# Optimization experiments

Hardware: AMD Instinct MI355X
Metric: run time of the kernel (lower is better)

Reference implementation:

```python
import jax, jax.numpy as jnp
import numpy as np

HIDDEN = 2048
N_HEADS = 16
HEAD_DIM = HIDDEN // N_HEADS  # 128
BATCH = 2
SEQ = 2048


def setup_inputs() -> dict:
    key = jax.random.key(0)
    ks = jax.random.split(key, 9)
    std = HIDDEN ** -0.5
    inp = {
        "hidden_states": jax.random.normal(ks[0], (BATCH, SEQ, HIDDEN), dtype=jnp.float32),
        "q_w": jax.random.normal(ks[1], (HIDDEN, HIDDEN), dtype=jnp.float32) * std,
        "k_w": jax.random.normal(ks[2], (HIDDEN, HIDDEN), dtype=jnp.float32) * std,
        "v_w": jax.random.normal(ks[3], (HIDDEN, HIDDEN), dtype=jnp.float32) * std,
        "o_w": jax.random.normal(ks[4], (HIDDEN, HIDDEN), dtype=jnp.float32) * std,
        "q_b": jnp.zeros((HIDDEN,), dtype=jnp.float32),
        "k_b": jnp.zeros((HIDDEN,), dtype=jnp.float32),
        "v_b": jnp.zeros((HIDDEN,), dtype=jnp.float32),
        "o_b": jnp.zeros((HIDDEN,), dtype=jnp.float32),
    }
    return inp


def reference(hidden_states, q_w, k_w, v_w, o_w, q_b, k_b, v_b, o_b):
    b, s, _ = hidden_states.shape
    # Projections (nn.Linear applies x @ W^T + b); split heads -> [b, h, s, d]
    def proj(w, bias):
        y = hidden_states @ w.T + bias
        return y.reshape(b, s, N_HEADS, HEAD_DIM).transpose(0, 2, 1, 3)

    q = proj(q_w, q_b)
    k = proj(k_w, k_b)
    v = proj(v_w, v_b)

    scale = 1.0 / jnp.sqrt(jnp.float32(HEAD_DIM))
    scores = jnp.einsum("bhqd,bhkd->bhqk", q, k) * scale  # [b, h, s, s]

    # causal mask: mask positions where k > q (triu, diagonal=1)
    qi = jnp.arange(s)[:, None]
    ki = jnp.arange(s)[None, :]
    scores = jnp.where(ki > qi, -jnp.inf, scores)

    attn = jax.nn.softmax(scores.astype(jnp.float32), axis=-1).astype(q.dtype)
    out = jnp.einsum("bhqk,bhkd->bhqd", attn, v)
    out = out.transpose(0, 2, 1, 3).reshape(b, s, HIDDEN)
    return out @ o_w.T + o_b
```

## Files before the change

### kernel.cpp

```cpp
#include <hip/hip_runtime.h>

#define S_HID 2048
#define S_SEQ 2048
#define S_B   2
#define S_NH  16
#define S_HD  128
#define S_M   (S_B * S_SEQ)
#define S_BH  (S_B * S_NH)

typedef __bf16 bf16_t;
typedef __bf16 bf16x8 __attribute__((ext_vector_type(8)));
typedef __bf16 bf16x4 __attribute__((ext_vector_type(4)));
typedef float  floatx4 __attribute__((ext_vector_type(4)));

typedef __attribute__((address_space(1))) unsigned int as1_uint;
typedef __attribute__((address_space(3))) unsigned int as3_uint;

__device__ __forceinline__ void gload_lds16(const void* g, void* l) {
    __builtin_amdgcn_global_load_lds((as1_uint*)g, (as3_uint*)l, 16, 0, 0);
}

__global__ void cvt_bf16(const float* __restrict__ src, bf16_t* __restrict__ dst, int n) {
    int nv = n >> 2;
    int stride = gridDim.x * blockDim.x;
    for (int i = blockIdx.x * blockDim.x + threadIdx.x; i < nv; i += stride) {
        float4 v = ((const float4*)src)[i];
        bf16x4 o;
        o.x = (bf16_t)v.x; o.y = (bf16_t)v.y; o.z = (bf16_t)v.z; o.w = (bf16_t)v.w;
        ((bf16x4*)dst)[i] = o;
    }
}

__global__ void transpose_v(const bf16_t* __restrict__ V, bf16_t* __restrict__ Vt) {
    __shared__ bf16_t tile[64 * 65];
    const int bh = blockIdx.z, s0 = blockIdx.y * 64, d0 = blockIdx.x * 64;
    const int t = threadIdx.x;
    #pragma unroll
    for (int i = 0; i < 16; ++i) {
        int idx = i * 256 + t;
        int r = idx >> 6, c = idx & 63;
        tile[r * 65 + c] = V[((size_t)bh * S_SEQ + s0 + r) * S_HD + d0 + c];
    }
    __syncthreads();
    #pragma unroll
    for (int i = 0; i < 16; ++i) {
        int idx = i * 256 + t;
        int rr = idx >> 6, cc = idx & 63;
        Vt[((size_t)bh * S_HD + d0 + rr) * S_SEQ + s0 + cc] = tile[cc * 65 + rr];
    }
}

__global__ __launch_bounds__(256, 2)
void gemm_bt(const bf16_t* __restrict__ A, const bf16_t* __restrict__ W,
             const float* __restrict__ bias, void* __restrict__ out,
             int mode, float scale) {
    __shared__ __align__(16) bf16_t ldsA[128 * 64];
    __shared__ __align__(16) bf16_t ldsB[128 * 64];
    const int tid = threadIdx.x;
    const int wid = tid >> 6, lane = tid & 63;
    const int m0 = blockIdx.y * 128, n0 = blockIdx.x * 128;
    const int wm = (wid & 1) * 64, wn = (wid >> 1) * 64;
    const int lm = lane & 15, quad = lane >> 4;
    const int srow = lane >> 3;
    const int scol = lane & 7;

    floatx4 acc[4][4];
    #pragma unroll
    for (int i = 0; i < 4; ++i)
        #pragma unroll
        for (int j = 0; j < 4; ++j)
            acc[i][j] = (floatx4){0.f, 0.f, 0.f, 0.f};

    for (int kt = 0; kt < S_HID; kt += 64) {
        #pragma unroll
        for (int i = 0; i < 4; ++i) {
            int slot = i * 4 + wid;
            int row = slot * 8 + srow;
            int cg = scol ^ (row & 7);
            gload_lds16(A + (size_t)(m0 + row) * S_HID + kt + cg * 8, &ldsA[slot * 512]);
            gload_lds16(W + (size_t)(n0 + row) * S_HID + kt + cg * 8, &ldsB[slot * 512]);
        }
        __syncthreads();
        #pragma unroll
        for (int k2 = 0; k2 < 2; ++k2) {
            bf16x8 af[4], bfr[4];
            #pragma unroll
            for (int i = 0; i < 4; ++i) {
                int row = wm + i * 16 + lm;
                int cc = (k2 * 4 + quad) ^ (row & 7);
                af[i] = *(const bf16x8*)&ldsA[row * 64 + cc * 8];
            }
            #pragma unroll
            for (int j = 0; j < 4; ++j) {
                int row = wn + j * 16 + lm;
                int cc = (k2 * 4 + quad) ^ (row & 7);
                bfr[j] = *(const bf16x8*)&ldsB[row * 64 + cc * 8];
            }
            #pragma unroll
            for (int i = 0; i < 4; ++i)
                #pragma unroll
                for (int j = 0; j < 4; ++j)
                    acc[i][j] = __builtin_amdgcn_mfma_f32_16x16x32_bf16(af[i], bfr[j], acc[i][j], 0, 0, 0);
        }
        __syncthreads();
    }

    if (mode == 0) {
        bf16_t* Ob = (bf16_t*)out;
        #pragma unroll
        for (int i = 0; i < 4; ++i) {
            #pragma unroll
            for (int j = 0; j < 4; ++j) {
                int n = n0 + wn + j * 16 + lm;
                float bv = bias[n];
                int h = n >> 7, d = n & 127;
                #pragma unroll
                for (int r = 0; r < 4; ++r) {
                    int m = m0 + wm + i * 16 + quad * 4 + r;
                    int b = m >> 11, s = m & 2047;
                    Ob[(((size_t)(b * S_NH + h)) * S_SEQ + s) * S_HD + d] =
                        (bf16_t)((acc[i][j][r] + bv) * scale);
                }
            }
        }
    } else {
        float* Of = (float*)out;
        #pragma unroll
        for (int i = 0; i < 4; ++i) {
            #pragma unroll
            for (int j = 0; j < 4; ++j) {
                int n = n0 + wn + j * 16 + lm;
                float bv = bias[n];
                #pragma unroll
                for (int r = 0; r < 4; ++r) {
                    int m = m0 + wm + i * 16 + quad * 4 + r;
                    Of[(size_t)m * S_HID + n] = acc[i][j][r] + bv;
                }
            }
        }
    }
}

__global__ __launch_bounds__(256, 2)
void attn(const bf16_t* __restrict__ Q, const bf16_t* __restrict__ K,
          const bf16_t* __restrict__ Vt, bf16_t* __restrict__ O) {
    __shared__ __align__(16) bf16_t ldsK[128 * 128];
    __shared__ __align__(16) bf16_t ldsV[128 * 128];
    __shared__ __align__(16) bf16_t ldsP[4 * 16 * 128];
    const int tid = threadIdx.x, wid = tid >> 6, lane = tid & 63;
    const int lm = lane & 15, quad = lane >> 4;
    const int pair = blockIdx.x;
    const int bh = blockIdx.y;
    const int b = bh >> 4, h = bh & 15;
    bf16_t* pb = &ldsP[wid * 2048];

    for (int seg = 0; seg < 2; ++seg) {
        const int q0 = seg ? (1984 - pair * 64) : (pair * 64);
        const int qrow = q0 + wid * 16 + lm;

        bf16x8 qf[4];
        {
            const bf16_t* qp = Q + ((size_t)bh * S_SEQ + qrow) * S_HD + quad * 8;
            #pragma unroll
            for (int ks = 0; ks < 4; ++ks) qf[ks] = *(const bf16x8*)(qp + ks * 32);
        }

        floatx4 oa[8];
        #pragma unroll
        for (int j = 0; j < 8; ++j) oa[j] = (floatx4){0.f, 0.f, 0.f, 0.f};
        float m_st = -1e30f, l_st = 0.f;

        const int nkt = (q0 + 64 + 127) >> 7;
        for (int kti = 0; kti < nkt; ++kti) {
            const int kt = kti * 128;
            #pragma unroll
            for (int i = 0; i < 8; ++i) {
                int slot = i * 4 + wid;
                int row = slot * 4 + quad;
                int cg = lm ^ (row & 7);
                gload_lds16(K + ((size_t)bh * S_SEQ + kt + row) * S_HD + cg * 8, &ldsK[slot * 512]);
                gload_lds16(Vt + ((size_t)bh * S_HD + row) * S_SEQ + kt + cg * 8, &ldsV[slot * 512]);
            }
            __syncthreads();

            floatx4 sa[8];
            #pragma unroll
            for (int j = 0; j < 8; ++j) sa[j] = (floatx4){0.f, 0.f, 0.f, 0.f};
            #pragma unroll
            for (int ks = 0; ks < 4; ++ks) {
                #pragma unroll
                for (int j = 0; j < 8; ++j) {
                    int row = j * 16 + lm;
                    int cc = (ks * 4 + quad) ^ (row & 7);
                    bf16x8 kb = *(const bf16x8*)&ldsK[row * 128 + cc * 8];
                    sa[j] = __builtin_amdgcn_mfma_f32_16x16x32_bf16(kb, qf[ks], sa[j], 0, 0, 0);
                }
            }
            if (kti == nkt - 1) {
                #pragma unroll
                for (int j = 0; j < 8; ++j)
                    #pragma unroll
                    for (int r = 0; r < 4; ++r) {
                        int key = kt + j * 16 + quad * 4 + r;
                        if (key > qrow) sa[j][r] = -1e30f;
                    }
            }
            float mx = sa[0][0];
            #pragma unroll
            for (int j = 0; j < 8; ++j)
                #pragma unroll
                for (int r = 0; r < 4; ++r) mx = fmaxf(mx, sa[j][r]);
            mx = fmaxf(mx, __shfl_xor(mx, 16));
            mx = fmaxf(mx, __shfl_xor(mx, 32));
            float mn = fmaxf(m_st, mx);
            float al = __builtin_amdgcn_exp2f(m_st - mn);
            m_st = mn;

            float rs = 0.f;
            #pragma unroll
            for (int j = 0; j < 8; ++j) {
                bf16x4 pk;
                #pragma unroll
                for (int r = 0; r < 4; ++r) {
                    float p = __builtin_amdgcn_exp2f(sa[j][r] - mn);
                    rs += p;
                    pk[r] = (bf16_t)p;
                }
                int pairidx = j * 2 + (quad >> 1);
                int chunk = ((pairidx ^ (lm & 7)) << 1) + (quad & 1);
                *(bf16x4*)&pb[lm * 128 + chunk * 4] = pk;
            }
            rs += __shfl_xor(rs, 16);
            rs += __shfl_xor(rs, 32);
            l_st = l_st * al + rs;
            #pragma unroll
            for (int j = 0; j < 8; ++j)
                #pragma unroll
                for (int r = 0; r < 4; ++r) oa[j][r] *= al;

            #pragma unroll
            for (int ks2 = 0; ks2 < 4; ++ks2) {
                int pr = (ks2 * 4 + quad) ^ (lm & 7);
                bf16x8 pf = *(const bf16x8*)&pb[lm * 128 + pr * 8];
                #pragma unroll
                for (int jd = 0; jd < 8; ++jd) {
                    int vrow = jd * 16 + lm;
                    int vc = (ks2 * 4 + quad) ^ (vrow & 7);
                    bf16x8 vb = *(const bf16x8*)&ldsV[vrow * 128 + vc * 8];
                    oa[jd] = __builtin_amdgcn_mfma_f32_16x16x32_bf16(vb, pf, oa[jd], 0, 0, 0);
                }
            }
            __syncthreads();
        }

        float inv = 1.0f / l_st;
        bf16_t* orow = O + ((size_t)b * S_SEQ + qrow) * S_HID + h * S_HD;
        #pragma unroll
        for (int jd = 0; jd < 8; ++jd) {
            bf16x4 ov;
            #pragma unroll
            for (int r = 0; r < 4; ++r) ov[r] = (bf16_t)(oa[jd][r] * inv);
            *(bf16x4*)&orow[jd * 16 + quad * 4] = ov;
        }
    }
}

extern "C" void kernel_launch(void* const* d_in, const int* in_sizes, int n_in,
                              void* d_out, int out_size, void* d_ws, size_t ws_size,
                              hipStream_t stream) {
    const float* hs = (const float*)d_in[0];
    const float* qw = (const float*)d_in[1];
    const float* kw = (const float*)d_in[2];
    const float* vw = (const float*)d_in[3];
    const float* ow = (const float*)d_in[4];
    const float* qbias = (const float*)d_in[5];
    const float* kbias = (const float*)d_in[6];
    const float* vbias = (const float*)d_in[7];
    const float* obias = (const float*)d_in[8];

    char* ws = (char*)d_ws;
    bf16_t* Xb  = (bf16_t*)(ws + 0);
    bf16_t* Wqb = (bf16_t*)(ws + 16777216);
    bf16_t* Wkb = (bf16_t*)(ws + 25165824);
    bf16_t* Wvb = (bf16_t*)(ws + 33554432);
    bf16_t* Wob = (bf16_t*)(ws + 41943040);
    bf16_t* Qb  = (bf16_t*)(ws + 50331648);
    bf16_t* Kb  = (bf16_t*)(ws + 67108864);
    bf16_t* Vb  = (bf16_t*)(ws + 83886080);
    bf16_t* Vtb = (bf16_t*)(ws + 100663296);
    bf16_t* Ob  = Xb;

    cvt_bf16<<<1024, 256, 0, stream>>>(hs, Xb, S_M * S_HID);
    cvt_bf16<<<512, 256, 0, stream>>>(qw, Wqb, S_HID * S_HID);
    cvt_bf16<<<512, 256, 0, stream>>>(kw, Wkb, S_HID * S_HID);
    cvt_bf16<<<512, 256, 0, stream>>>(vw, Wvb, S_HID * S_HID);
    cvt_bf16<<<512, 256, 0, stream>>>(ow, Wob, S_HID * S_HID);

    dim3 gg(S_HID / 128, S_M / 128);
    const float qscale = 0.08838834764831845f * 1.4426950408889634f;
    gemm_bt<<<gg, 256, 0, stream>>>(Xb, Wqb, qbias, (void*)Qb, 0, qscale);
    gemm_bt<<<gg, 256, 0, stream>>>(Xb, Wkb, kbias, (void*)Kb, 0, 1.0f);
    gemm_bt<<<gg, 256, 0, stream>>>(Xb, Wvb, vbias, (void*)Vb, 0, 1.0f);

    transpose_v<<<dim3(2, 32, 32), 256, 0, stream>>>(Vb, Vtb);

    attn<<<dim3(16, S_BH), 256, 0, stream>>>(Qb, Kb, Vtb, Ob);

    gemm_bt<<<gg, 256, 0, stream>>>(Ob, Wob, obias, d_out, 1, 1.0f);
}
```

Before: 417.5 us.

## Rewrite attention with 32x32 MFMA, double-buffered K/V, register P, fused V transpose

The attention kernel now uses 32x32x16 MFMA tiles with 128-query blocks. K/V tiles are double-buffered in LDS so the next tile's loads overlap compute, and the P fragments are built in registers via cross-lane shuffles instead of a round trip through LDS. The V projection GEMM writes V already transposed, which removes the separate transpose kernel and its extra memory traffic. In exchange, LDS use grows to 128KB, occupancy drops to one block per CU, and the grid shrinks to 256 blocks, which may leave some CUs underused.

```diff
diff --git a/kernel.cpp b/kernel.cpp
--- a/kernel.cpp
+++ b/kernel.cpp
@@ -12,6 +12,7 @@
 typedef __bf16 bf16x8 __attribute__((ext_vector_type(8)));
 typedef __bf16 bf16x4 __attribute__((ext_vector_type(4)));
 typedef float  floatx4 __attribute__((ext_vector_type(4)));
+typedef float  floatx16 __attribute__((ext_vector_type(16)));
 
 typedef __attribute__((address_space(1))) unsigned int as1_uint;
 typedef __attribute__((address_space(3))) unsigned int as3_uint;
@@ -28,25 +29,6 @@
         bf16x4 o;
         o.x = (bf16_t)v.x; o.y = (bf16_t)v.y; o.z = (bf16_t)v.z; o.w = (bf16_t)v.w;
         ((bf16x4*)dst)[i] = o;
-    }
-}
-
-__global__ void transpose_v(const bf16_t* __restrict__ V, bf16_t* __restrict__ Vt) {
-    __shared__ bf16_t tile[64 * 65];
-    const int bh = blockIdx.z, s0 = blockIdx.y * 64, d0 = blockIdx.x * 64;
-    const int t = threadIdx.x;
-    #pragma unroll
-    for (int i = 0; i < 16; ++i) {
-        int idx = i * 256 + t;
-        int r = idx >> 6, c = idx & 63;
-        tile[r * 65 + c] = V[((size_t)bh * S_SEQ + s0 + r) * S_HD + d0 + c];
-    }
-    __syncthreads();
-    #pragma unroll
-    for (int i = 0; i < 16; ++i) {
-        int idx = i * 256 + t;
-        int rr = idx >> 6, cc = idx & 63;
-        Vt[((size_t)bh * S_HD + d0 + rr) * S_SEQ + s0 + cc] = tile[cc * 65 + rr];
     }
 }
 
@@ -123,7 +105,7 @@
                 }
             }
         }
-    } else {
+    } else if (mode == 1) {
         float* Of = (float*)out;
         #pragma unroll
         for (int i = 0; i < 4; ++i) {
@@ -138,130 +120,184 @@
                 }
             }
         }
+    } else {
+        bf16_t* Vt = (bf16_t*)out;
+        #pragma unroll
+        for (int i = 0; i < 4; ++i) {
+            #pragma unroll
+            for (int j = 0; j < 4; ++j) {
+                int n = n0 + wn + j * 16 + lm;
+                float bv = bias[n];
+                int h = n >> 7, d = n & 127;
+                int m = m0 + wm + i * 16 + quad * 4;
+                int b = m >> 11, s = m & 2047;
+                bf16x4 ov;
+                #pragma unroll
+                for (int r = 0; r < 4; ++r) ov[r] = (bf16_t)(acc[i][j][r] + bv);
+                *(bf16x4*)&Vt[(((size_t)(b * S_NH + h)) * S_HD + d) * S_SEQ + s] = ov;
+            }
+        }
     }
 }
 
-__global__ __launch_bounds__(256, 2)
+__device__ __forceinline__ bf16x8 make_pfrag(bf16x4 lo, bf16x4 hi, int h) {
+    int2 li = __builtin_bit_cast(int2, lo);
+    int2 hh = __builtin_bit_cast(int2, hi);
+    int2 xl, xh;
+    xl.x = __shfl_xor(li.x, 32); xl.y = __shfl_xor(li.y, 32);
+    xh.x = __shfl_xor(hh.x, 32); xh.y = __shfl_xor(hh.y, 32);
+    int2 flo, fhi;
+    flo.x = h ? xh.x : li.x;  flo.y = h ? xh.y : li.y;
+    fhi.x = h ? hh.x : xl.x;  fhi.y = h ? hh.y : xl.y;
+    bf16x4 a = __builtin_bit_cast(bf16x4, flo);
+    bf16x4 b = __builtin_bit_cast(bf16x4, fhi);
+    return __builtin_shufflevector(a, b, 0, 1, 2, 3, 4, 5, 6, 7);
+}
+
+__global__ __launch_bounds__(256, 1)
 void attn(const bf16_t* __restrict__ Q, const bf16_t* __restrict__ K,
           const bf16_t* __restrict__ Vt, bf16_t* __restrict__ O) {
-    __shared__ __align__(16) bf16_t ldsK[128 * 128];
-    __shared__ __align__(16) bf16_t ldsV[128 * 128];
-    __shared__ __align__(16) bf16_t ldsP[4 * 16 * 128];
+    __shared__ __align__(16) bf16_t ldsK[2][128 * 128];
+    __shared__ __align__(16) bf16_t ldsV[2][128 * 128];
     const int tid = threadIdx.x, wid = tid >> 6, lane = tid & 63;
     const int lm = lane & 15, quad = lane >> 4;
-    const int pair = blockIdx.x;
-    const int bh = blockIdx.y;
-    const int b = bh >> 4, h = bh & 15;
-    bf16_t* pb = &ldsP[wid * 2048];
-
+    const int c31 = lane & 31, h = lane >> 5, r7 = lane & 7;
+    const int bx = blockIdx.x;
+    const int bh = bx & 31, pair = bx >> 5;
+    const int b = bh >> 4, hd = bh & 15;
+
+    const bf16_t* Kbase = K + (size_t)bh * S_SEQ * S_HD;
+    const bf16_t* Vbase = Vt + (size_t)bh * S_HD * S_SEQ;
+
+    int pp = 0;
+    #pragma unroll
     for (int seg = 0; seg < 2; ++seg) {
-        const int q0 = seg ? (1984 - pair * 64) : (pair * 64);
-        const int qrow = q0 + wid * 16 + lm;
-
-        bf16x8 qf[4];
+        const int q0 = seg ? (1920 - pair * 128) : (pair * 128);
+        const int qcol = q0 + wid * 32 + c31;
+        const int nkt = (q0 >> 7) + 1;
+
+        bf16x8 qf[8];
         {
-            const bf16_t* qp = Q + ((size_t)bh * S_SEQ + qrow) * S_HD + quad * 8;
-            #pragma unroll
-            for (int ks = 0; ks < 4; ++ks) qf[ks] = *(const bf16x8*)(qp + ks * 32);
-        }
-
-        floatx4 oa[8];
-        #pragma unroll
-        for (int j = 0; j < 8; ++j) oa[j] = (floatx4){0.f, 0.f, 0.f, 0.f};
+            const bf16_t* qp = Q + ((size_t)bh * S_SEQ + qcol) * S_HD + h * 8;
+            #pragma unroll
+            for (int ks = 0; ks < 8; ++ks) qf[ks] = *(const bf16x8*)(qp + ks * 16);
+        }
+
+        floatx16 oa[4];
+        #pragma unroll
+        for (int jd = 0; jd < 4; ++jd)
+            #pragma unroll
+            for (int e = 0; e < 16; ++e) oa[jd][e] = 0.f;
         float m_st = -1e30f, l_st = 0.f;
 
-        const int nkt = (q0 + 64 + 127) >> 7;
-        for (int kti = 0; kti < nkt; ++kti) {
-            const int kt = kti * 128;
+        {
             #pragma unroll
             for (int i = 0; i < 8; ++i) {
                 int slot = i * 4 + wid;
                 int row = slot * 4 + quad;
                 int cg = lm ^ (row & 7);
-                gload_lds16(K + ((size_t)bh * S_SEQ + kt + row) * S_HD + cg * 8, &ldsK[slot * 512]);
-                gload_lds16(Vt + ((size_t)bh * S_HD + row) * S_SEQ + kt + cg * 8, &ldsV[slot * 512]);
-            }
+                gload_lds16(Kbase + (size_t)row * S_HD + cg * 8, &ldsK[pp][slot * 512]);
+                gload_lds16(Vbase + (size_t)row * S_SEQ + cg * 8, &ldsV[pp][slot * 512]);
+            }
+        }
+
+        for (int kti = 0; kti < nkt; ++kti) {
+            const int kt = kti * 128;
             __syncthreads();
 
-            floatx4 sa[8];
-            #pragma unroll
-            for (int j = 0; j < 8; ++j) sa[j] = (floatx4){0.f, 0.f, 0.f, 0.f};
-            #pragma unroll
-            for (int ks = 0; ks < 4; ++ks) {
-                #pragma unroll
-                for (int j = 0; j < 8; ++j) {
-                    int row = j * 16 + lm;
-                    int cc = (ks * 4 + quad) ^ (row & 7);
-                    bf16x8 kb = *(const bf16x8*)&ldsK[row * 128 + cc * 8];
-                    sa[j] = __builtin_amdgcn_mfma_f32_16x16x32_bf16(kb, qf[ks], sa[j], 0, 0, 0);
-                }
-            }
+            if (kti + 1 < nkt) {
+                const int ktn = kt + 128;
+                #pragma unroll
+                for (int i = 0; i < 8; ++i) {
+                    int slot = i * 4 + wid;
+                    int row = slot * 4 + quad;
+                    int cg = lm ^ (row & 7);
+                    gload_lds16(Kbase + (size_t)(ktn + row) * S_HD + cg * 8, &ldsK[pp ^ 1][slot * 512]);
+                    gload_lds16(Vbase + (size_t)row * S_SEQ + ktn + cg * 8, &ldsV[pp ^ 1][slot * 512]);
+                }
+            }
+
+            floatx16 sa[4];
+            #pragma unroll
+            for (int jr = 0; jr < 4; ++jr)
+                #pragma unroll
+                for (int e = 0; e < 16; ++e) sa[jr][e] = 0.f;
+            #pragma unroll
+            for (int ks = 0; ks < 8; ++ks) {
+                #pragma unroll
+                for (int jr = 0; jr < 4; ++jr) {
+                    int row = jr * 32 + c31;
+                    bf16x8 kf = *(const bf16x8*)&ldsK[pp][row * 128 + (((ks * 2 + h) ^ r7)) * 8];
+                    sa[jr] = __builtin_amdgcn_mfma_f32_32x32x16_bf16(kf, qf[ks], sa[jr], 0, 0, 0);
+                }
+            }
+
             if (kti == nkt - 1) {
                 #pragma unroll
-                for (int j = 0; j < 8; ++j)
+                for (int jr = 0; jr < 4; ++jr)
                     #pragma unroll
-                    for (int r = 0; r < 4; ++r) {
-                        int key = kt + j * 16 + quad * 4 + r;
-                        if (key > qrow) sa[j][r] = -1e30f;
+                    for (int rr = 0; rr < 16; ++rr) {
+                        int key = kt + jr * 32 + (rr & 3) + 8 * (rr >> 2) + 4 * h;
+                        if (key > qcol) sa[jr][rr] = -1e30f;
                     }
             }
-            float mx = sa[0][0];
-            #pragma unroll
-            for (int j = 0; j < 8; ++j)
-                #pragma unroll
-                for (int r = 0; r < 4; ++r) mx = fmaxf(mx, sa[j][r]);
-            mx = fmaxf(mx, __shfl_xor(mx, 16));
+
+            float mx = -1e30f;
+            #pragma unroll
+            for (int jr = 0; jr < 4; ++jr)
+                #pragma unroll
+                for (int rr = 0; rr < 16; ++rr) mx = fmaxf(mx, sa[jr][rr]);
             mx = fmaxf(mx, __shfl_xor(mx, 32));
             float mn = fmaxf(m_st, mx);
             float al = __builtin_amdgcn_exp2f(m_st - mn);
             m_st = mn;
 
             float rs = 0.f;
-            #pragma unroll
-            for (int j = 0; j < 8; ++j) {
-                bf16x4 pk;
-                #pragma unroll
-                for (int r = 0; r < 4; ++r) {
-                    float p = __builtin_amdgcn_exp2f(sa[j][r] - mn);
-                    rs += p;
-                    pk[r] = (bf16_t)p;
-                }
-                int pairidx = j * 2 + (quad >> 1);
-                int chunk = ((pairidx ^ (lm & 7)) << 1) + (quad & 1);
-                *(bf16x4*)&pb[lm * 128 + chunk * 4] = pk;
-            }
-            rs += __shfl_xor(rs, 16);
+            bf16x8 pf[8];
+            #pragma unroll
+            for (int jr = 0; jr < 4; ++jr) {
+                bf16x4 pk[4];
+                #pragma unroll
+                for (int g = 0; g < 4; ++g)
+                    #pragma unroll
+                    for (int e = 0; e < 4; ++e) {
+                        float p = __builtin_amdgcn_exp2f(sa[jr][g * 4 + e] - mn);
+                        rs += p;
+                        pk[g][e] = (bf16_t)p;
+                    }
+                pf[jr * 2]     = make_pfrag(pk[0], pk[1], h);
+                pf[jr * 2 + 1] = make_pfrag(pk[2], pk[3], h);
+            }
             rs += __shfl_xor(rs, 32);
             l_st = l_st * al + rs;
             #pragma unroll
-            for (int j = 0; j < 8; ++j)
-                #pragma unroll
-                for (int r = 0; r < 4; ++r) oa[j][r] *= al;
-
-            #pragma unroll
-            for (int ks2 = 0; ks2 < 4; ++ks2) {
-                int pr = (ks2 * 4 + quad) ^ (lm & 7);
-                bf16x8 pf = *(const bf16x8*)&pb[lm * 128 + pr * 8];
-                #pragma unroll
-                for (int jd = 0; jd < 8; ++jd) {
-                    int vrow = jd * 16 + lm;
-                    int vc = (ks2 * 4 + quad) ^ (vrow & 7);
-                    bf16x8 vb = *(const bf16x8*)&ldsV[vrow * 128 + vc * 8];
-                    oa[jd] = __builtin_amdgcn_mfma_f32_16x16x32_bf16(vb, pf, oa[jd], 0, 0, 0);
-                }
-            }
-            __syncthreads();
+            for (int jd = 0; jd < 4; ++jd)
+                #pragma unroll
+                for (int e = 0; e < 16; ++e) oa[jd][e] *= al;
+
+            #pragma unroll
+            for (int kb = 0; kb < 8; ++kb) {
+                #pragma unroll
+                for (int jd = 0; jd < 4; ++jd) {
+                    int row = jd * 32 + c31;
+                    bf16x8 vf = *(const bf16x8*)&ldsV[pp][row * 128 + (((kb * 2 + h) ^ r7)) * 8];
+                    oa[jd] = __builtin_amdgcn_mfma_f32_32x32x16_bf16(vf, pf[kb], oa[jd], 0, 0, 0);
+                }
+            }
+            pp ^= 1;
         }
 
         float inv = 1.0f / l_st;
-        bf16_t* orow = O + ((size_t)b * S_SEQ + qrow) * S_HID + h * S_HD;
-        #pragma unroll
-        for (int jd = 0; jd < 8; ++jd) {
-            bf16x4 ov;
-            #pragma unroll
-            for (int r = 0; r < 4; ++r) ov[r] = (bf16_t)(oa[jd][r] * inv);
-            *(bf16x4*)&orow[jd * 16 + quad * 4] = ov;
-        }
+        bf16_t* op = O + ((size_t)b * S_SEQ + qcol) * S_HID + hd * S_HD;
+        #pragma unroll
+        for (int jd = 0; jd < 4; ++jd)
+            #pragma unroll
+            for (int g = 0; g < 4; ++g) {
+                bf16x4 ov;
+                #pragma unroll
+                for (int e = 0; e < 4; ++e) ov[e] = (bf16_t)(oa[jd][g * 4 + e] * inv);
+                *(bf16x4*)&op[jd * 32 + g * 8 + 4 * h] = ov;
+            }
     }
 }
 
@@ -286,8 +322,7 @@
     bf16_t* Wob = (bf16_t*)(ws + 41943040);
     bf16_t* Qb  = (bf16_t*)(ws + 50331648);
     bf16_t* Kb  = (bf16_t*)(ws + 67108864);
-    bf16_t* Vb  = (bf16_t*)(ws + 83886080);
-    bf16_t* Vtb = (bf16_t*)(ws + 100663296);
+    bf16_t* Vtb = (bf16_t*)(ws + 83886080);
     bf16_t* Ob  = Xb;
 
     cvt_bf16<<<1024, 256, 0, stream>>>(hs, Xb, S_M * S_HID);
@@ -300,11 +335,9 @@
     const float qscale = 0.08838834764831845f * 1.4426950408889634f;
     gemm_bt<<<gg, 256, 0, stream>>>(Xb, Wqb, qbias, (void*)Qb, 0, qscale);
     gemm_bt<<<gg, 256, 0, stream>>>(Xb, Wkb, kbias, (void*)Kb, 0, 1.0f);
-    gemm_bt<<<gg, 256, 0, stream>>>(Xb, Wvb, vbias, (void*)Vb, 0, 1.0f);
-
-    transpose_v<<<dim3(2, 32, 32), 256, 0, stream>>>(Vb, Vtb);
-
-    attn<<<dim3(16, S_BH), 256, 0, stream>>>(Qb, Kb, Vtb, Ob);
+    gemm_bt<<<gg, 256, 0, stream>>>(Xb, Wvb, vbias, (void*)Vtb, 2, 1.0f);
+
+    attn<<<256, 256, 0, stream>>>(Qb, Kb, Vtb, Ob);
 
     gemm_bt<<<gg, 256, 0, stream>>>(Ob, Wob, obias, d_out, 1, 1.0f);
 }
```

Measured after the change: 380.7 us. 1.1x faster.
